# Kernel optimization log

Measured on AMD Instinct MI355X. Metric: run time of the kernel, lower is better.

## Reference

```python
import jax, jax.numpy as jnp
import numpy as np

T, B = 256, 512
IN, NG = 512, 5
H, LAT = 2048, 1024


def gru_cell(x, h, w_ih, w_hh, b_ih, b_hh):
    # torch.nn.GRUCell math
    gi = x @ w_ih.T + b_ih            # [B, 3H]
    gh = h @ w_hh.T + b_hh            # [B, 3H]
    ir, iz, inn = jnp.split(gi, 3, axis=-1)
    hr, hz, hn = jnp.split(gh, 3, axis=-1)
    r = jax.nn.sigmoid(ir + hr)
    z = jax.nn.sigmoid(iz + hz)
    n = jnp.tanh(inn + r * hn)
    return (1.0 - z) * n + z * h


def setup_inputs() -> dict:
    key = jax.random.key(0)
    ks = jax.random.split(key, 20)
    s = 0.02
    d = {
        "x": jax.random.normal(ks[0], (T, B, IN + NG), jnp.float32),
        "latent_genre_vec": jax.random.uniform(ks[1], (B, NG), jnp.float32),
        "eps": jax.random.normal(ks[2], (B, LAT - NG), jnp.float32),
        "enc_w_ih": s * jax.random.normal(ks[3], (3 * H, IN + NG), jnp.float32),
        "enc_w_hh": s * jax.random.normal(ks[4], (3 * H, H), jnp.float32),
        "enc_b_ih": jnp.zeros((3 * H,), jnp.float32),
        "enc_b_hh": jnp.zeros((3 * H,), jnp.float32),
        "dec_w_ih": s * jax.random.normal(ks[5], (3 * H, IN), jnp.float32),
        "dec_w_hh": s * jax.random.normal(ks[6], (3 * H, H), jnp.float32),
        "dec_b_ih": jnp.zeros((3 * H,), jnp.float32),
        "dec_b_hh": jnp.zeros((3 * H,), jnp.float32),
        "fc_mu_w": s * jax.random.normal(ks[7], (LAT - NG, H), jnp.float32),
        "fc_mu_b": jnp.zeros((LAT - NG,), jnp.float32),
        "fc_logvar_w": s * jax.random.normal(ks[8], (LAT - NG, H), jnp.float32),
        "fc_logvar_b": jnp.zeros((LAT - NG,), jnp.float32),
        "fc_output_w": s * jax.random.normal(ks[9], (H, LAT), jnp.float32),
        "fc_output_b": jnp.zeros((H,), jnp.float32),
        "fc_decoder_w": s * jax.random.normal(ks[10], (IN, H), jnp.float32),
        "fc_decoder_b": jnp.zeros((IN,), jnp.float32),
    }
    return d


def reference(x, latent_genre_vec, eps,
              enc_w_ih, enc_w_hh, enc_b_ih, enc_b_hh,
              dec_w_ih, dec_w_hh, dec_b_ih, dec_b_hh,
              fc_mu_w, fc_mu_b, fc_logvar_w, fc_logvar_b,
              fc_output_w, fc_output_b, fc_decoder_w, fc_decoder_b):
    Bsz = x.shape[1]
    h0 = jnp.zeros((Bsz, enc_w_hh.shape[1]), x.dtype)

    # encoder: sequential GRU over time
    def enc_step(h, xt):
        return gru_cell(xt, h, enc_w_ih, enc_w_hh, enc_b_ih, enc_b_hh), None
    h_enc, _ = jax.lax.scan(enc_step, h0, x)

    mu = h_enc @ fc_mu_w.T + fc_mu_b
    logvar = h_enc @ fc_logvar_w.T + fc_logvar_b
    z = mu + jnp.exp(0.5 * logvar) * eps
    z = jnp.concatenate((z, latent_genre_vec), axis=1)
    h_dec0 = z @ fc_output_w.T + fc_output_b

    note0 = jnp.zeros((Bsz, fc_decoder_w.shape[0]), x.dtype)

    def dec_step(carry, _):
        h, note = carry
        h = gru_cell(note, h, dec_w_ih, dec_w_hh, dec_b_ih, dec_b_hh)
        note = h @ fc_decoder_w.T + fc_decoder_b
        return (h, note), note

    _, output = jax.lax.scan(dec_step, (h_dec0, note0), None, length=x.shape[0])
    return output, mu, logvar
```

## Files before the change

kernel.cpp:

```cpp
#include <hip/hip_runtime.h>
#include <hip/hip_bf16.h>

typedef __bf16 bf16_t;
typedef bf16_t bfx8 __attribute__((ext_vector_type(8)));
typedef float  fx4  __attribute__((ext_vector_type(4)));

#define TT     256
#define BB     512
#define INDIM  512
#define NGENRE 5
#define HD     2048
#define LATD   1024
#define LATM   1019
#define XK     517
#define XKP    576
#define CHUNK  64

__device__ __forceinline__ bf16_t f2b(float f) {
  unsigned u = __builtin_bit_cast(unsigned, f);
  u += 0x7fffu + ((u >> 16) & 1u);
  unsigned short s = (unsigned short)(u >> 16);
  return __builtin_bit_cast(bf16_t, s);
}
__device__ __forceinline__ float sigmoidf_(float x) { return 1.0f / (1.0f + __expf(-x)); }

__device__ __forceinline__ void gload16(const bf16_t* g, bf16_t* l) {
  __builtin_amdgcn_global_load_lds((const __attribute__((address_space(1))) void*)g,
                                   (__attribute__((address_space(3))) void*)l,
                                   16, 0, 0);
}
__device__ __forceinline__ void wait_vm0()  { asm volatile("s_waitcnt vmcnt(0)" ::: "memory"); }
__device__ __forceinline__ void wait_vm4()  { asm volatile("s_waitcnt vmcnt(4)" ::: "memory"); }
__device__ __forceinline__ void wait_vm5()  { asm volatile("s_waitcnt vmcnt(5)" ::: "memory"); }
__device__ __forceinline__ void wait_vm6()  { asm volatile("s_waitcnt vmcnt(6)" ::: "memory"); }
__device__ __forceinline__ void wait_vm10() { asm volatile("s_waitcnt vmcnt(10)" ::: "memory"); }
__device__ __forceinline__ void wait_vm12() { asm volatile("s_waitcnt vmcnt(12)" ::: "memory"); }
__device__ __forceinline__ void wait_lgkm0() { asm volatile("s_waitcnt lgkmcnt(0)" ::: "memory"); }

__global__ void wcast_pad(const float* __restrict__ src, bf16_t* __restrict__ dst,
                          int rows_src, int rows_pad, int K, int ldp) {
  for (int r = blockIdx.x; r < rows_pad; r += gridDim.x)
    for (int c = threadIdx.x; c < ldp; c += 256)
      dst[(size_t)r * ldp + c] = (r < rows_src && c < K) ? f2b(src[(size_t)r * K + c]) : f2b(0.0f);
}

__global__ void wtransp(const float* __restrict__ src, bf16_t* __restrict__ dst) {
  int i = blockIdx.x * 256 + threadIdx.x;
  int r = i >> 9, c = i & 511;
  dst[i] = f2b(src[(size_t)c * 2048 + r]);
}
__global__ void bcomp(const float* __restrict__ wih, const float* __restrict__ bdec,
                      float* __restrict__ bc) {
  int r = blockIdx.x * 256 + threadIdx.x;
  if (r >= 3 * HD) return;
  float s = 0.f;
  for (int k = 0; k < 512; ++k) s += wih[(size_t)r * 512 + k] * bdec[k];
  bc[r] = s;
}
__global__ void biasbuild(const float* __restrict__ bc, const float* __restrict__ bih,
                          const float* __restrict__ bhh,
                          float4* __restrict__ bD, float4* __restrict__ bD0) {
  int c = blockIdx.x * 256 + threadIdx.x;
  if (c >= HD) return;
  float r0 = bih[c] + bhh[c];
  float z0 = bih[HD + c] + bhh[HD + c];
  float i0 = bih[2 * HD + c];
  float h0 = bhh[2 * HD + c];
  bD0[c] = float4{r0, z0, i0, h0};
  bD[c]  = float4{r0 + bc[c], z0 + bc[HD + c], i0 + bc[2 * HD + c], h0};
}
__global__ void wprime(const bf16_t* __restrict__ wc, const bf16_t* __restrict__ whh,
                       bf16_t* __restrict__ wp, bf16_t* __restrict__ wp0) {
  const size_t total = (size_t)4 * HD * HD;
  for (size_t i = (size_t)blockIdx.x * 256 + threadIdx.x; i < total; i += (size_t)gridDim.x * 256) {
    int row = (int)(i >> 11), k = (int)(i & 2047);
    int g = row >> 11, j = row & 2047;
    bf16_t v, v0;
    if (g == 0) {
      float a = (float)wc[(size_t)j * HD + k], b = (float)whh[(size_t)j * HD + k];
      v = f2b(a + b); v0 = whh[(size_t)j * HD + k];
    } else if (g == 1) {
      size_t o = (size_t)(HD + j) * HD + k;
      v = f2b((float)wc[o] + (float)whh[o]); v0 = whh[o];
    } else if (g == 2) {
      v = wc[(size_t)(2 * HD + j) * HD + k]; v0 = f2b(0.0f);
    } else {
      v = whh[(size_t)(2 * HD + j) * HD + k]; v0 = v;
    }
    wp[i] = v; wp0[i] = v0;
  }
}

__global__ __launch_bounds__(256, 2)
void gruC(const bf16_t* __restrict__ Hb,
          const bf16_t* __restrict__ Wp,
          const float4* __restrict__ bias4,
          const float* __restrict__ Hin,
          float* __restrict__ Hout, bf16_t* __restrict__ HoutB)
{
  __shared__ bf16_t aT[3][64 * 64];
  __shared__ bf16_t bT[3][128 * 64];
  const int tid = threadIdx.x, wv = tid >> 6, lane = tid & 63;
  const int bid = blockIdx.x;
  const int j0 = (bid & 63) * 32;
  const int m0 = (bid >> 6) * 64;
  const int lr = lane & 15, lk = lane >> 4;
  const int rl = lane >> 3;
  const int cl = (lane & 7) * 8;

  fx4 acc[2][4];
#pragma unroll
  for (int fj = 0; fj < 2; ++fj)
#pragma unroll
    for (int g = 0; g < 4; ++g) acc[fj][g] = fx4{0.f, 0.f, 0.f, 0.f};

  int aOff[2], aSlot[2];
#pragma unroll
  for (int i = 0; i < 2; ++i) {
    const int t = wv * 2 + i;
    const int r = t * 8 + rl;
    const int c = cl ^ ((r & 7) * 8);
    aOff[i] = (m0 + r) * HD + c;
    aSlot[i] = t * 512;
  }
  int bOff[4], bSlot[4];
#pragma unroll
  for (int i = 0; i < 4; ++i) {
    const int t = wv * 4 + i;
    const int r = t * 8 + rl;
    const int g = r >> 5, jj = r & 31;
    const int c = cl ^ ((r & 7) * 8);
    bOff[i] = (g * HD + j0 + jj) * HD + c;
    bSlot[i] = t * 512;
  }
  int aRow, bRow[4][2], ko[2];
  aRow = (wv * 16 + lr) * 64;
#pragma unroll
  for (int g = 0; g < 4; ++g)
#pragma unroll
    for (int fj = 0; fj < 2; ++fj) bRow[g][fj] = (g * 32 + fj * 16 + lr) * 64;
#pragma unroll
  for (int h = 0; h < 2; ++h) ko[h] = (h * 32 + lk * 8) ^ ((lr & 7) * 8);

  auto stage = [&](int buf, int s) {
    const int kb = s * 64;
#pragma unroll
    for (int i = 0; i < 2; ++i) gload16(Hb + aOff[i] + kb, &aT[buf][aSlot[i]]);
#pragma unroll
    for (int i = 0; i < 4; ++i) gload16(Wp + bOff[i] + kb, &bT[buf][bSlot[i]]);
  };

  const int nk = HD / 64;
  stage(0, 0); stage(1, 1);
  int rb = 0, sb = 2;
  for (int s = 0; s < nk; ++s) {
    if (s == nk - 1) wait_vm0(); else wait_vm6();
    __builtin_amdgcn_s_barrier();
    if (s + 2 < nk) stage(sb, s + 2);
    const bf16_t* aB = &aT[rb][0];
    const bf16_t* bB = &bT[rb][0];
    bfx8 af[2]; bfx8 bfr[4][2][2];
#pragma unroll
    for (int h = 0; h < 2; ++h)
      af[h] = *reinterpret_cast<const bfx8*>(&aB[aRow + ko[h]]);
#pragma unroll
    for (int g = 0; g < 4; ++g)
#pragma unroll
      for (int fj = 0; fj < 2; ++fj)
#pragma unroll
        for (int h = 0; h < 2; ++h)
          bfr[g][fj][h] = *reinterpret_cast<const bfx8*>(&bB[bRow[g][fj] + ko[h]]);
    wait_lgkm0();
    __builtin_amdgcn_sched_barrier(0);
    __builtin_amdgcn_s_setprio(1);
#pragma unroll
    for (int h = 0; h < 2; ++h)
#pragma unroll
      for (int g = 0; g < 4; ++g)
#pragma unroll
        for (int fj = 0; fj < 2; ++fj)
          acc[fj][g] = __builtin_amdgcn_mfma_f32_16x16x32_bf16(af[h], bfr[g][fj][h], acc[fj][g], 0, 0, 0);
    __builtin_amdgcn_s_setprio(0);
    rb = (rb == 2) ? 0 : rb + 1;
    sb = (sb == 2) ? 0 : sb + 1;
  }

#pragma unroll
  for (int fj = 0; fj < 2; ++fj) {
    const int col = j0 + fj * 16 + lr;
    const float4 bb = bias4[col];
    const int rbase = m0 + wv * 16 + lk * 4;
#pragma unroll
    for (int q = 0; q < 4; ++q) {
      const int row = rbase + q;
      const float r = sigmoidf_(acc[fj][0][q] + bb.x);
      const float z = sigmoidf_(acc[fj][1][q] + bb.y);
      const float n = tanhf(acc[fj][2][q] + bb.z + r * (acc[fj][3][q] + bb.w));
      const float hv = (1.0f - z) * n + z * Hin[(size_t)row * HD + col];
      Hout[(size_t)row * HD + col]  = hv;
      HoutB[(size_t)row * HD + col] = f2b(hv);
    }
  }
}

__global__ __launch_bounds__(256, 2)
void gru6(const bf16_t* __restrict__ A1, int lda1, int k1s,
          const bf16_t* __restrict__ Wih, int ldwih,
          const bf16_t* __restrict__ Hb,
          const bf16_t* __restrict__ Whh,
          const float* __restrict__ Hin,
          const float* __restrict__ bih, const float* __restrict__ bhh,
          float* __restrict__ Hout, bf16_t* __restrict__ HoutB)
{
  __shared__ bf16_t aT[3][128 * 64];
  __shared__ bf16_t bT[3][48 * 64];
  const int tid = threadIdx.x, wv = tid >> 6, lane = tid & 63;
  const int bid = blockIdx.x;
  const int xcd = bid & 7, loc = bid >> 3;
  const int j0 = (xcd * 16 + (loc >> 2)) * 16;
  const int m0 = (loc & 3) * 128;
  const int lr = lane & 15, lk = lane >> 4;
  const int rl = lane >> 3;
  const int cl = (lane & 7) * 8;

  fx4 acc[2][4];
#pragma unroll
  for (int m = 0; m < 2; ++m)
#pragma unroll
    for (int g = 0; g < 4; ++g) acc[m][g] = fx4{0.f, 0.f, 0.f, 0.f};

  const bf16_t* A1b = A1 ? A1 : Hb;

  int aOff0[4], aOff1[4], aSlot[4];
#pragma unroll
  for (int i = 0; i < 4; ++i) {
    const int t = wv * 4 + i;
    const int r = t * 8 + rl;
    const int c = cl ^ ((r & 7) * 8);
    aOff0[i] = (m0 + r) * lda1 + c;
    aOff1[i] = (m0 + r) * HD + c;
    aSlot[i] = t * 512;
  }
  const int nB  = (wv < 2) ? 2 : 1;
  const int bt0 = (wv < 2) ? wv * 2 : (2 + wv);
  int bOff0[2], bOff1[2], bSlot[2];
#pragma unroll
  for (int i = 0; i < 2; ++i) {
    const int t = bt0 + (i < nB ? i : 0);
    const int r = t * 8 + rl;
    const int g = r >> 4, jj = r & 15;
    const int c = cl ^ ((r & 7) * 8);
    bOff0[i] = (g * HD + j0 + jj) * ldwih + c;
    bOff1[i] = (g * HD + j0 + jj) * HD + c;
    bSlot[i] = t * 512;
  }
  int aRow[2], bRow[3], ko[2];
#pragma unroll
  for (int m = 0; m < 2; ++m) aRow[m] = (wv * 32 + m * 16 + lr) * 64;
#pragma unroll
  for (int g = 0; g < 3; ++g) bRow[g] = (g * 16 + lr) * 64;
#pragma unroll
  for (int h = 0; h < 2; ++h) ko[h] = (h * 32 + lk * 8) ^ ((lr & 7) * 8);

  auto stage = [&](int buf, int s) {
    const bool p = (s >= k1s);
    const int kb = (p ? (s - k1s) : s) * 64;
    bf16_t* aD = &aT[buf][0];
    bf16_t* bD = &bT[buf][0];
    if (p) {
#pragma unroll
      for (int i = 0; i < 4; ++i) gload16(Hb + aOff1[i] + kb, aD + aSlot[i]);
      gload16(Whh + bOff1[0] + kb, bD + bSlot[0]);
      if (wv < 2) gload16(Whh + bOff1[1] + kb, bD + bSlot[1]);
    } else {
#pragma unroll
      for (int i = 0; i < 4; ++i) gload16(A1b + aOff0[i] + kb, aD + aSlot[i]);
      gload16(Wih + bOff0[0] + kb, bD + bSlot[0]);
      if (wv < 2) gload16(Wih + bOff0[1] + kb, bD + bSlot[1]);
    }
  };

  const int nk = k1s + HD / 64;
  stage(0, 0); stage(1, 1); stage(2, 2);
  int buf = 0;
  for (int s = 0; s < nk; ++s) {
    const int rem = nk - 1 - s;
    if (rem >= 2)      { if (wv < 2) wait_vm12(); else wait_vm10(); }
    else if (rem == 1) { if (wv < 2) wait_vm6();  else wait_vm5();  }
    else               wait_vm0();
    __builtin_amdgcn_s_barrier();
    const bf16_t* aB = &aT[buf][0];
    const bf16_t* bB = &bT[buf][0];
    bfx8 af[2][2], bfr[3][2];
#pragma unroll
    for (int m = 0; m < 2; ++m)
#pragma unroll
      for (int h = 0; h < 2; ++h)
        af[m][h] = *reinterpret_cast<const bfx8*>(&aB[aRow[m] + ko[h]]);
#pragma unroll
    for (int g = 0; g < 3; ++g)
#pragma unroll
      for (int h = 0; h < 2; ++h)
        bfr[g][h] = *reinterpret_cast<const bfx8*>(&bB[bRow[g] + ko[h]]);
    wait_lgkm0();
    __builtin_amdgcn_sched_barrier(0);
    __builtin_amdgcn_s_barrier();
    if (s + 3 < nk) stage(buf, s + 3);
    const bool p = (s >= k1s);
    __builtin_amdgcn_s_setprio(1);
#pragma unroll
    for (int h = 0; h < 2; ++h)
#pragma unroll
      for (int g = 0; g < 3; ++g) {
        const int slot = (g == 2) ? (p ? 3 : 2) : g;
#pragma unroll
        for (int m = 0; m < 2; ++m)
          acc[m][slot] = __builtin_amdgcn_mfma_f32_16x16x32_bf16(af[m][h], bfr[g][h], acc[m][slot], 0, 0, 0);
      }
    __builtin_amdgcn_s_setprio(0);
    buf = (buf == 2) ? 0 : buf + 1;
  }

  const int col = j0 + lr;
  const float br  = bih[col] + bhh[col];
  const float bz  = bih[HD + col] + bhh[HD + col];
  const float bin = bih[2 * HD + col];
  const float bhn = bhh[2 * HD + col];
#pragma unroll
  for (int m = 0; m < 2; ++m) {
    const int rbase = m0 + wv * 32 + m * 16 + lk * 4;
#pragma unroll
    for (int q = 0; q < 4; ++q) {
      const int row = rbase + q;
      const float r = sigmoidf_(acc[m][0][q] + br);
      const float z = sigmoidf_(acc[m][1][q] + bz);
      const float n = tanhf(acc[m][2][q] + bin + r * (acc[m][3][q] + bhn));
      const float hv = (1.0f - z) * n + z * Hin[(size_t)row * HD + col];
      Hout[(size_t)row * HD + col]  = hv;
      HoutB[(size_t)row * HD + col] = f2b(hv);
    }
  }
}

__global__ __launch_bounds__(256, 2)
void gemm_nt3(const bf16_t* __restrict__ A, int lda, int K,
              const bf16_t* __restrict__ W, int ldw,
              const float* __restrict__ bias,
              float* __restrict__ O, int ldo, int N,
              bf16_t* __restrict__ OB, int ldob)
{
  __shared__ bf16_t aT[2][64 * 64];
  __shared__ bf16_t bT[2][64 * 64];
  const int tid = threadIdx.x, wave = tid >> 6, lane = tid & 63;
  const int m0 = blockIdx.y * 64, n0 = blockIdx.x * 64;
  const int wm = wave & 1, wn = wave >> 1;
  const int lr = lane & 15, lk = lane >> 4;
  const int rl = lane >> 3, cl = (lane & 7) * 8;

  fx4 acc[2][2];
#pragma unroll
  for (int a = 0; a < 2; ++a)
#pragma unroll
    for (int b = 0; b < 2; ++b) acc[a][b] = fx4{0.f, 0.f, 0.f, 0.f};

  const bf16_t* pA[2]; const bf16_t* pB[2]; int slot[2];
#pragma unroll
  for (int i = 0; i < 2; ++i) {
    const int t = wave * 2 + i;
    const int r = t * 8 + rl;
    const int c = cl ^ ((r & 7) * 8);
    pA[i] = A + (size_t)(m0 + r) * lda + c;
    pB[i] = W + (size_t)(n0 + r) * ldw + c;
    slot[i] = t * 512;
  }
  int aRow[2], bRow[2], ko[2];
#pragma unroll
  for (int f = 0; f < 2; ++f) {
    aRow[f] = (wm * 32 + f * 16 + lr) * 64;
    bRow[f] = (wn * 32 + f * 16 + lr) * 64;
  }
#pragma unroll
  for (int h = 0; h < 2; ++h) ko[h] = (h * 32 + lk * 8) ^ ((lr & 7) * 8);

  auto stage = [&](int buf, int kb) {
#pragma unroll
    for (int i = 0; i < 2; ++i) {
      gload16(pA[i] + kb, &aT[buf][slot[i]]);
      gload16(pB[i] + kb, &bT[buf][slot[i]]);
    }
  };

  const int nk = K >> 6;
  stage(0, 0);
  stage(1, 64);
  for (int s = 0; s < nk; ++s) {
    if (s == nk - 1) wait_vm0(); else wait_vm4();
    __builtin_amdgcn_s_barrier();
    const bf16_t* aB = &aT[s & 1][0];
    const bf16_t* bB = &bT[s & 1][0];
    bfx8 af[2][2], bfr[2][2];
#pragma unroll
    for (int f = 0; f < 2; ++f)
#pragma unroll
      for (int h = 0; h < 2; ++h) {
        af[f][h]  = *reinterpret_cast<const bfx8*>(&aB[aRow[f] + ko[h]]);
        bfr[f][h] = *reinterpret_cast<const bfx8*>(&bB[bRow[f] + ko[h]]);
      }
    wait_lgkm0();
    __builtin_amdgcn_sched_barrier(0);
    __builtin_amdgcn_s_barrier();
    if (s + 2 < nk) stage(s & 1, (s + 2) << 6);
    __builtin_amdgcn_s_setprio(1);
#pragma unroll
    for (int h = 0; h < 2; ++h)
#pragma unroll
      for (int fm = 0; fm < 2; ++fm)
#pragma unroll
        for (int fj = 0; fj < 2; ++fj)
          acc[fm][fj] = __builtin_amdgcn_mfma_f32_16x16x32_bf16(af[fm][h], bfr[fj][h], acc[fm][fj], 0, 0, 0);
    __builtin_amdgcn_s_setprio(0);
  }

#pragma unroll
  for (int fm = 0; fm < 2; ++fm)
#pragma unroll
    for (int fj = 0; fj < 2; ++fj) {
      const int col = n0 + wn * 32 + fj * 16 + lr;
      if (col < N) {
        const float bb = bias[col];
#pragma unroll
        for (int q = 0; q < 4; ++q) {
          const int row = m0 + wm * 32 + fm * 16 + lk * 4 + q;
          const float v = acc[fm][fj][q] + bb;
          O[(size_t)row * ldo + col] = v;
          if (OB) OB[(size_t)row * ldob + col] = f2b(v);
        }
      }
    }
}

__global__ void build_zb(const float* __restrict__ mu, const float* __restrict__ lv,
                         const float* __restrict__ eps, const float* __restrict__ genre,
                         bf16_t* __restrict__ zb) {
  int i = blockIdx.x * 256 + threadIdx.x;
  int b = i >> 10, c = i & 1023;
  float v;
  if (c < LATM) {
    size_t k = (size_t)b * LATM + c;
    v = mu[k] + expf(0.5f * lv[k]) * eps[k];
  } else {
    v = genre[b * NGENRE + (c - LATM)];
  }
  zb[i] = f2b(v);
}

__global__ __launch_bounds__(256, 1)
void gru_stepF(const float* __restrict__ A1, int lda1, int K1,
               const float* __restrict__ Wih,
               const float* __restrict__ Hin,
               const float* __restrict__ Whh,
               const float* __restrict__ bih, const float* __restrict__ bhh,
               float* __restrict__ Hout)
{
  __shared__ bf16_t a_lds[128][32];
  __shared__ bf16_t b_lds[96][32];
  const int tid = threadIdx.x, wave = tid >> 6, lane = tid & 63;
  const int m0 = (blockIdx.x >> 6) * 128, j0 = (blockIdx.x & 63) * 32;
  const int lr = lane & 15, lk = lane >> 4;
  fx4 acc[2][2][4];
#pragma unroll
  for (int a = 0; a < 2; ++a)
#pragma unroll
    for (int b = 0; b < 2; ++b)
#pragma unroll
      for (int g = 0; g < 4; ++g) acc[a][b][g] = fx4{0.f, 0.f, 0.f, 0.f};

  for (int ph = 0; ph < 2; ++ph) {
    const float* Ag = ph ? Hin : A1;
    const int lda = ph ? HD : lda1, kLen = ph ? HD : K1;
    const float* W = ph ? Whh : Wih;
    const int nslot = ph ? 3 : 2;
    const int nkk = (kLen + 31) >> 5;
    for (int s = 0; s < nkk; ++s) {
      const int kb = s << 5;
#pragma unroll
      for (int it = 0; it < 16; ++it) {
        int i = tid + it * 256;
        int r = i >> 5, kk = i & 31, gk = kb + kk;
        float v = 0.0f;
        if (Ag && gk < kLen) v = Ag[(size_t)(m0 + r) * lda + gk];
        a_lds[r][kk] = f2b(v);
      }
#pragma unroll
      for (int it = 0; it < 12; ++it) {
        int i = tid + it * 256;
        int r = i >> 5, kk = i & 31, g = r >> 5, jj = r & 31, gk = kb + kk;
        b_lds[r][kk] = (gk < kLen) ? f2b(W[(size_t)(g * HD + j0 + jj) * kLen + gk]) : f2b(0.0f);
      }
      __syncthreads();
      bfx8 af[2];
#pragma unroll
      for (int fm = 0; fm < 2; ++fm)
        af[fm] = *reinterpret_cast<const bfx8*>(&a_lds[wave * 32 + fm * 16 + lr][lk * 8]);
#pragma unroll
      for (int g = 0; g < 3; ++g) {
        const int slot = (g == 2) ? nslot : g;
#pragma unroll
        for (int fj = 0; fj < 2; ++fj) {
          bfx8 bfr = *reinterpret_cast<const bfx8*>(&b_lds[g * 32 + fj * 16 + lr][lk * 8]);
#pragma unroll
          for (int fm = 0; fm < 2; ++fm)
            acc[fm][fj][slot] = __builtin_amdgcn_mfma_f32_16x16x32_bf16(af[fm], bfr, acc[fm][fj][slot], 0, 0, 0);
        }
      }
      __syncthreads();
    }
  }
#pragma unroll
  for (int fj = 0; fj < 2; ++fj) {
    const int col = j0 + fj * 16 + lr;
    const float br = bih[col] + bhh[col];
    const float bz = bih[HD + col] + bhh[HD + col];
    const float bin = bih[2 * HD + col];
    const float bhn = bhh[2 * HD + col];
#pragma unroll
    for (int fm = 0; fm < 2; ++fm) {
      const int rbase = m0 + wave * 32 + fm * 16 + lk * 4;
#pragma unroll
      for (int q = 0; q < 4; ++q) {
        const int row = rbase + q;
        const float r = sigmoidf_(acc[fm][fj][0][q] + br);
        const float z = sigmoidf_(acc[fm][fj][1][q] + bz);
        const float n = tanhf(acc[fm][fj][2][q] + bin + r * (acc[fm][fj][3][q] + bhn));
        Hout[(size_t)row * HD + col] = (1.0f - z) * n + z * Hin[(size_t)row * HD + col];
      }
    }
  }
}

__global__ __launch_bounds__(256, 1)
void gemm_ntF(const float* __restrict__ A, int lda, int K,
              const float* __restrict__ W,
              const float* __restrict__ bias,
              float* __restrict__ O, int ldo, int N)
{
  __shared__ bf16_t a_lds[64][32];
  __shared__ bf16_t b_lds[64][32];
  const int tid = threadIdx.x, wave = tid >> 6, lane = tid & 63;
  const int m0 = blockIdx.y * 64, n0 = blockIdx.x * 64;
  const int wm = (wave & 1) * 32, wn = (wave >> 1) * 32;
  const int lr = lane & 15, lk = lane >> 4;
  fx4 acc[2][2];
#pragma unroll
  for (int a = 0; a < 2; ++a)
#pragma unroll
    for (int b = 0; b < 2; ++b) acc[a][b] = fx4{0.f, 0.f, 0.f, 0.f};
  for (int kb = 0; kb < K; kb += 32) {
#pragma unroll
    for (int it = 0; it < 8; ++it) {
      int i = tid + it * 256;
      int r = i >> 5, kk = i & 31;
      a_lds[r][kk] = f2b(A[(size_t)(m0 + r) * lda + kb + kk]);
    }
#pragma unroll
    for (int it = 0; it < 8; ++it) {
      int i = tid + it * 256;
      int r = i >> 5, kk = i & 31;
      int n = n0 + r;
      b_lds[r][kk] = (n < N) ? f2b(W[(size_t)n * K + kb + kk]) : f2b(0.0f);
    }
    __syncthreads();
    bfx8 af[2], bfr[2];
#pragma unroll
    for (int f = 0; f < 2; ++f) {
      af[f] = *reinterpret_cast<const bfx8*>(&a_lds[wm + f * 16 + lr][lk * 8]);
      bfr[f] = *reinterpret_cast<const bfx8*>(&b_lds[wn + f * 16 + lr][lk * 8]);
    }
#pragma unroll
    for (int fm = 0; fm < 2; ++fm)
#pragma unroll
      for (int fj = 0; fj < 2; ++fj)
        acc[fm][fj] = __builtin_amdgcn_mfma_f32_16x16x32_bf16(af[fm], bfr[fj], acc[fm][fj], 0, 0, 0);
    __syncthreads();
  }
#pragma unroll
  for (int fm = 0; fm < 2; ++fm)
#pragma unroll
    for (int fj = 0; fj < 2; ++fj) {
      const int col = n0 + wn + fj * 16 + lr;
      if (col < N) {
        const float bb = bias[col];
#pragma unroll
        for (int q = 0; q < 4; ++q) {
          const int row = m0 + wm + fm * 16 + lk * 4 + q;
          O[(size_t)row * ldo + col] = acc[fm][fj][q] + bb;
        }
      }
    }
}

__global__ void build_zf(const float* __restrict__ mu, const float* __restrict__ lv,
                         const float* __restrict__ eps, const float* __restrict__ genre,
                         float* __restrict__ z) {
  int i = blockIdx.x * 256 + threadIdx.x;
  int b = i >> 10, c = i & 1023;
  z[i] = (c < LATM) ? mu[(size_t)b * LATM + c] + expf(0.5f * lv[(size_t)b * LATM + c]) * eps[(size_t)b * LATM + c]
                    : genre[b * NGENRE + (c - LATM)];
}

extern "C" void kernel_launch(void* const* d_in, const int* in_sizes, int n_in,
                              void* d_out, int out_size, void* d_ws, size_t ws_size,
                              hipStream_t stream) {
  const float* x      = (const float*)d_in[0];
  const float* genre  = (const float*)d_in[1];
  const float* eps    = (const float*)d_in[2];
  const float* eWih   = (const float*)d_in[3];
  const float* eWhh   = (const float*)d_in[4];
  const float* eBih   = (const float*)d_in[5];
  const float* eBhh   = (const float*)d_in[6];
  const float* dWih   = (const float*)d_in[7];
  const float* dWhh   = (const float*)d_in[8];
  const float* dBih   = (const float*)d_in[9];
  const float* dBhh   = (const float*)d_in[10];
  const float* fcMuW  = (const float*)d_in[11];
  const float* fcMuB  = (const float*)d_in[12];
  const float* fcLvW  = (const float*)d_in[13];
  const float* fcLvB  = (const float*)d_in[14];
  const float* fcOutW = (const float*)d_in[15];
  const float* fcOutB = (const float*)d_in[16];
  const float* fcDecW = (const float*)d_in[17];
  const float* fcDecB = (const float*)d_in[18];

  float* out = (float*)d_out;
  float* muO = out + (size_t)TT * BB * INDIM;
  float* lvO = muO + (size_t)BB * LATM;

  const size_t nEih = (size_t)3 * HD * XKP;
  const size_t nEhh = (size_t)3 * HD * HD;
  const size_t nDih = (size_t)3 * HD * INDIM;
  const size_t nDhh = (size_t)3 * HD * HD;
  const size_t nMu  = (size_t)1024 * HD;
  const size_t nOut = (size_t)HD * LATD;
  const size_t nDec = (size_t)INDIM * HD;
  const size_t oEih = 0;
  const size_t oEhh = oEih + nEih;
  const size_t oDih = oEhh + nEhh;
  const size_t oDhh = oDih + nDih;
  const size_t oMu  = oDhh + nDhh;
  const size_t oLv  = oMu + nMu;
  const size_t oOut = oLv + nMu;
  const size_t oDec = oOut + nOut;
  const size_t wTot = oDec + nDec;

  const size_t bytesW  = wTot * 2;
  const size_t bytesHF = (size_t)BB * HD * 4;
  const size_t bytesHB = (size_t)BB * HD * 2;
  const size_t bytesZB = (size_t)BB * LATD * 2;
  const size_t bytesNB = (size_t)BB * INDIM * 2;
  const size_t bytesX1 = (size_t)BB * XKP * 2;
  const size_t bytesXB = (size_t)TT * BB * XKP * 2;
  const size_t needB = bytesW + 2 * bytesHF + 2 * bytesHB + bytesZB + bytesNB + bytesX1 + 1024;
  const size_t needA = needB + bytesXB;
  const size_t bytesWdT  = (size_t)HD * 512 * 2;
  const size_t bytesWcB  = (size_t)3 * HD * HD * 2;
  const size_t bytesWcF  = (size_t)3 * HD * HD * 4;
  const size_t bytesWp   = (size_t)4 * HD * HD * 2;
  const size_t bytesBc   = (size_t)3 * HD * 4;
  const size_t bytesB4   = (size_t)HD * 16;
  const size_t bytesZero = (size_t)HD * 4;
  const size_t bytesHist = (size_t)CHUNK * BB * HD * 2;
  const size_t needC = needA + bytesWdT + bytesWcB + bytesWcF + 2 * bytesWp +
                       bytesBc + 2 * bytesB4 + bytesZero + bytesHist + 1024;

  if (ws_size >= needB) {
    const bool haveXB = (ws_size >= needA);
    const bool haveCP = (ws_size >= needC);
    char* p = (char*)d_ws;
    bf16_t* wb = (bf16_t*)p;            p += bytesW;
    float* h0  = (float*)p;             p += bytesHF;
    float* h1  = (float*)p;             p += bytesHF;
    bf16_t* hb0 = (bf16_t*)p;           p += bytesHB;
    bf16_t* hb1 = (bf16_t*)p;           p += bytesHB;
    bf16_t* zb  = (bf16_t*)p;           p += bytesZB;
    bf16_t* nb  = (bf16_t*)p;           p += bytesNB;
    bf16_t* x1  = (bf16_t*)p;           p += bytesX1;
    bf16_t* xb  = haveXB ? (bf16_t*)p : nullptr;
    if (haveXB) p += bytesXB;
    bf16_t *wdT = nullptr, *wcB = nullptr, *wP = nullptr, *wP0 = nullptr, *hist = nullptr;
    float *wcF = nullptr, *bc = nullptr, *zerosb = nullptr;
    float4 *b4D = nullptr, *b4D0 = nullptr;
    if (haveCP) {
      wdT = (bf16_t*)p;  p += bytesWdT;
      wcB = (bf16_t*)p;  p += bytesWcB;
      wP  = (bf16_t*)p;  p += bytesWp;
      wP0 = (bf16_t*)p;  p += bytesWp;
      wcF = (float*)p;   p += bytesWcF;
      bc  = (float*)p;   p += bytesBc;
      b4D = (float4*)p;  p += bytesB4;
      b4D0 = (float4*)p; p += bytesB4;
      zerosb = (float*)p; p += bytesZero;
      hist = (bf16_t*)p; p += bytesHist;
    }

    auto cast = [&](const float* s, bf16_t* d, int rs, int rp, int K, int ldp) {
      int g = rp > 8192 ? 8192 : rp;
      wcast_pad<<<g, 256, 0, stream>>>(s, d, rs, rp, K, ldp);
    };
    cast(eWih,   wb + oEih, 3 * HD, 3 * HD, XK,    XKP);
    cast(eWhh,   wb + oEhh, 3 * HD, 3 * HD, HD,    HD);
    cast(dWih,   wb + oDih, 3 * HD, 3 * HD, INDIM, INDIM);
    cast(dWhh,   wb + oDhh, 3 * HD, 3 * HD, HD,    HD);
    cast(fcMuW,  wb + oMu,  LATM,   1024,   HD,    HD);
    cast(fcLvW,  wb + oLv,  LATM,   1024,   HD,    HD);
    cast(fcOutW, wb + oOut, HD,     HD,     LATD,  LATD);
    cast(fcDecW, wb + oDec, INDIM,  INDIM,  HD,    HD);
    if (haveXB) cast(x, xb, TT * BB, TT * BB, XK, XKP);

    if (haveCP) {
      hipMemsetAsync(zerosb, 0, bytesZero, stream);
      wtransp<<<(HD * 512) / 256, 256, 0, stream>>>(fcDecW, wdT);
      gemm_nt3<<<dim3(HD / 64, (3 * HD) / 64), 256, 0, stream>>>(
          wb + oDih, INDIM, INDIM, wdT, INDIM, zerosb, wcF, HD, HD, wcB, HD);
      bcomp<<<(3 * HD) / 256, 256, 0, stream>>>(dWih, fcDecB, bc);
      biasbuild<<<HD / 256, 256, 0, stream>>>(bc, dBih, dBhh, b4D, b4D0);
      wprime<<<4096, 256, 0, stream>>>(wcB, wb + oDhh, wP, wP0);
    }

    hipMemsetAsync(h0, 0, bytesHF, stream);
    hipMemsetAsync(hb0, 0, bytesHB, stream);

    float*  hF[2] = {h0, h1};
    bf16_t* hB[2] = {hb0, hb1};

    for (int t = 0; t < TT; ++t) {
      const int ci = t & 1, co = ci ^ 1;
      const bf16_t* xt;
      if (haveXB) {
        xt = xb + (size_t)t * BB * XKP;
      } else {
        wcast_pad<<<512, 256, 0, stream>>>(x + (size_t)t * BB * XK, x1, BB, BB, XK, XKP);
        xt = x1;
      }
      gru6<<<512, 256, 0, stream>>>(xt, XKP, XKP / 64,
                                    wb + oEih, XKP, hB[ci], wb + oEhh,
                                    hF[ci], eBih, eBhh, hF[co], hB[co]);
    }
    gemm_nt3<<<dim3(16, 8), 256, 0, stream>>>(hB[0], HD, HD, wb + oMu, HD, fcMuB,
                                              muO, LATM, LATM, nullptr, 0);
    gemm_nt3<<<dim3(16, 8), 256, 0, stream>>>(hB[0], HD, HD, wb + oLv, HD, fcLvB,
                                              lvO, LATM, LATM, nullptr, 0);
    build_zb<<<(BB * LATD) / 256, 256, 0, stream>>>(muO, lvO, eps, genre, zb);
    gemm_nt3<<<dim3(32, 8), 256, 0, stream>>>(zb, LATD, LATD, wb + oOut, LATD, fcOutB,
                                              hF[0], HD, HD, hB[0], HD);
    if (haveCP) {
      for (int t = 0; t < TT; ++t) {
        const bf16_t* hprev = (t == 0) ? hB[0] : hist + (size_t)((t - 1) & (CHUNK - 1)) * BB * HD;
        gruC<<<512, 256, 0, stream>>>(hprev, t ? wP : wP0, t ? b4D : b4D0,
                                      hF[t & 1], hF[(t & 1) ^ 1],
                                      hist + (size_t)(t & (CHUNK - 1)) * BB * HD);
        if ((t & (CHUNK - 1)) == CHUNK - 1) {
          gemm_nt3<<<dim3(INDIM / 64, (CHUNK * BB) / 64), 256, 0, stream>>>(
              hist, HD, HD, wb + oDec, HD, fcDecB,
              out + (size_t)(t - (CHUNK - 1)) * BB * INDIM, INDIM, INDIM, nullptr, 0);
        }
      }
    } else {
      for (int t = 0; t < TT; ++t) {
        const int ci = t & 1, co = ci ^ 1;
        gru6<<<512, 256, 0, stream>>>(t ? nb : (const bf16_t*)nullptr, INDIM,
                                      t ? INDIM / 64 : 0,
                                      wb + oDih, INDIM, hB[ci], wb + oDhh,
                                      hF[ci], dBih, dBhh, hF[co], hB[co]);
        gemm_nt3<<<dim3(8, 8), 256, 0, stream>>>(hB[co], HD, HD, wb + oDec, HD, fcDecB,
                                                 out + (size_t)t * BB * INDIM, INDIM, INDIM,
                                                 nb, INDIM);
      }
    }
  } else {
    float* h0 = (float*)d_ws;
    float* h1 = h0 + (size_t)BB * HD;
    float* zb = h1 + (size_t)BB * HD;
    hipMemsetAsync(h0, 0, (size_t)BB * HD * sizeof(float), stream);
    float* hF[2] = {h0, h1};
    for (int t = 0; t < TT; ++t) {
      const int ci = t & 1, co = ci ^ 1;
      gru_stepF<<<256, 256, 0, stream>>>(x + (size_t)t * BB * XK, XK, XK, eWih,
                                         hF[ci], eWhh, eBih, eBhh, hF[co]);
    }
    gemm_ntF<<<dim3(16, 8), 256, 0, stream>>>(hF[0], HD, HD, fcMuW, fcMuB, muO, LATM, LATM);
    gemm_ntF<<<dim3(16, 8), 256, 0, stream>>>(hF[0], HD, HD, fcLvW, fcLvB, lvO, LATM, LATM);
    build_zf<<<(BB * LATD) / 256, 256, 0, stream>>>(muO, lvO, eps, genre, zb);
    gemm_ntF<<<dim3(32, 8), 256, 0, stream>>>(zb, LATD, LATD, fcOutW, fcOutB, hF[0], HD, HD);
    for (int t = 0; t < TT; ++t) {
      const int ci = t & 1, co = ci ^ 1;
      gru_stepF<<<256, 256, 0, stream>>>(t ? out + (size_t)(t - 1) * BB * INDIM : nullptr,
                                         INDIM, INDIM, dWih, hF[ci], dWhh, dBih, dBhh, hF[co]);
      gemm_ntF<<<dim3(8, 8), 256, 0, stream>>>(hF[co], HD, HD, fcDecW, fcDecB,
                                               out + (size_t)t * BB * INDIM, INDIM, INDIM);
    }
  }
  (void)in_sizes; (void)n_in; (void)out_size;
}
```

Before: 17.12 ms.

## Precompute encoder input projections in one GEMM and retile decoder GRU kernel

Hoists the encoder's x@W_ih projection out of the time loop into a single large batched GEMM whose bf16 results are stored in the workspace. A new per-step kernel then only multiplies by W_hh and adds the precomputed gates. The decoder recurrent kernel is also retiled so each wave owns output columns rather than rows, with the gate epilogue staged through LDS. The encoder path needs a large extra workspace and stores the input gates in bf16.

New measurement: 17.04 ms. No clear change (-0.4%).

```diff
diff --git a/kernel.cpp b/kernel.cpp
--- a/kernel.cpp
+++ b/kernel.cpp
@@ -15,6 +15,7 @@
 #define XK     517
 #define XKP    576
 #define CHUNK  64
+#define GIW    6144
 
 __device__ __forceinline__ bf16_t f2b(float f) {
   unsigned u = __builtin_bit_cast(unsigned, f);
@@ -92,11 +93,11 @@
 }
 
 __global__ __launch_bounds__(256, 2)
-void gruC(const bf16_t* __restrict__ Hb,
-          const bf16_t* __restrict__ Wp,
-          const float4* __restrict__ bias4,
-          const float* __restrict__ Hin,
-          float* __restrict__ Hout, bf16_t* __restrict__ HoutB)
+void gruC2(const bf16_t* __restrict__ Hb,
+           const bf16_t* __restrict__ Wp,
+           const float4* __restrict__ bias4,
+           const float* __restrict__ Hin,
+           float* __restrict__ Hout, bf16_t* __restrict__ HoutB)
 {
   __shared__ bf16_t aT[3][64 * 64];
   __shared__ bf16_t bT[3][128 * 64];
@@ -108,11 +109,11 @@
   const int rl = lane >> 3;
   const int cl = (lane & 7) * 8;
 
-  fx4 acc[2][4];
-#pragma unroll
-  for (int fj = 0; fj < 2; ++fj)
-#pragma unroll
-    for (int g = 0; g < 4; ++g) acc[fj][g] = fx4{0.f, 0.f, 0.f, 0.f};
+  fx4 acc[4][2];
+#pragma unroll
+  for (int m = 0; m < 4; ++m)
+#pragma unroll
+    for (int fj = 0; fj < 2; ++fj) acc[m][fj] = fx4{0.f, 0.f, 0.f, 0.f};
 
   int aOff[2], aSlot[2];
 #pragma unroll
@@ -133,12 +134,11 @@
     bOff[i] = (g * HD + j0 + jj) * HD + c;
     bSlot[i] = t * 512;
   }
-  int aRow, bRow[4][2], ko[2];
-  aRow = (wv * 16 + lr) * 64;
-#pragma unroll
-  for (int g = 0; g < 4; ++g)
-#pragma unroll
-    for (int fj = 0; fj < 2; ++fj) bRow[g][fj] = (g * 32 + fj * 16 + lr) * 64;
+  int aRow[4], bRow[2], ko[2];
+#pragma unroll
+  for (int m = 0; m < 4; ++m) aRow[m] = (m * 16 + lr) * 64;
+#pragma unroll
+  for (int fj = 0; fj < 2; ++fj) bRow[fj] = (wv * 32 + fj * 16 + lr) * 64;
 #pragma unroll
   for (int h = 0; h < 2; ++h) ko[h] = (h * 32 + lk * 8) ^ ((lr & 7) * 8);
 
@@ -159,46 +159,181 @@
     if (s + 2 < nk) stage(sb, s + 2);
     const bf16_t* aB = &aT[rb][0];
     const bf16_t* bB = &bT[rb][0];
-    bfx8 af[2]; bfx8 bfr[4][2][2];
-#pragma unroll
-    for (int h = 0; h < 2; ++h)
-      af[h] = *reinterpret_cast<const bfx8*>(&aB[aRow + ko[h]]);
-#pragma unroll
-    for (int g = 0; g < 4; ++g)
-#pragma unroll
-      for (int fj = 0; fj < 2; ++fj)
-#pragma unroll
-        for (int h = 0; h < 2; ++h)
-          bfr[g][fj][h] = *reinterpret_cast<const bfx8*>(&bB[bRow[g][fj] + ko[h]]);
+    bfx8 af[4][2], bfr[2][2];
+#pragma unroll
+    for (int m = 0; m < 4; ++m)
+#pragma unroll
+      for (int h = 0; h < 2; ++h)
+        af[m][h] = *reinterpret_cast<const bfx8*>(&aB[aRow[m] + ko[h]]);
+#pragma unroll
+    for (int fj = 0; fj < 2; ++fj)
+#pragma unroll
+      for (int h = 0; h < 2; ++h)
+        bfr[fj][h] = *reinterpret_cast<const bfx8*>(&bB[bRow[fj] + ko[h]]);
     wait_lgkm0();
     __builtin_amdgcn_sched_barrier(0);
     __builtin_amdgcn_s_setprio(1);
 #pragma unroll
     for (int h = 0; h < 2; ++h)
 #pragma unroll
-      for (int g = 0; g < 4; ++g)
+      for (int m = 0; m < 4; ++m)
 #pragma unroll
         for (int fj = 0; fj < 2; ++fj)
-          acc[fj][g] = __builtin_amdgcn_mfma_f32_16x16x32_bf16(af[h], bfr[g][fj][h], acc[fj][g], 0, 0, 0);
+          acc[m][fj] = __builtin_amdgcn_mfma_f32_16x16x32_bf16(af[m][h], bfr[fj][h], acc[m][fj], 0, 0, 0);
     __builtin_amdgcn_s_setprio(0);
     rb = (rb == 2) ? 0 : rb + 1;
     sb = (sb == 2) ? 0 : sb + 1;
   }
 
-#pragma unroll
-  for (int fj = 0; fj < 2; ++fj) {
-    const int col = j0 + fj * 16 + lr;
-    const float4 bb = bias4[col];
-    const int rbase = m0 + wv * 16 + lk * 4;
+  __syncthreads();
+  float* eL = (float*)&bT[0][0];
+#pragma unroll
+  for (int m = 0; m < 4; ++m)
+#pragma unroll
+    for (int fj = 0; fj < 2; ++fj)
+#pragma unroll
+      for (int q = 0; q < 4; ++q)
+        eL[((wv * 64 + m * 16 + lk * 4 + q) * 33 + fj * 16 + lr)] = acc[m][fj][q];
+  __syncthreads();
+  const int col = lane & 31;
+  const int rh  = lane >> 5;
+  const float4 bb = bias4[j0 + col];
+#pragma unroll
+  for (int i = 0; i < 8; ++i) {
+    const int rowL = wv * 16 + rh * 8 + i;
+    const float e0 = eL[((0 * 64 + rowL) * 33 + col)];
+    const float e1 = eL[((1 * 64 + rowL) * 33 + col)];
+    const float e2 = eL[((2 * 64 + rowL) * 33 + col)];
+    const float e3 = eL[((3 * 64 + rowL) * 33 + col)];
+    const float r = sigmoidf_(e0 + bb.x);
+    const float z = sigmoidf_(e1 + bb.y);
+    const float n = tanhf(e2 + bb.z + r * (e3 + bb.w));
+    const size_t o = (size_t)(m0 + rowL) * HD + j0 + col;
+    const float hv = (1.0f - z) * n + z * Hin[o];
+    Hout[o]  = hv;
+    HoutB[o] = f2b(hv);
+  }
+}
+
+__global__ __launch_bounds__(256, 2)
+void gruE(const bf16_t* __restrict__ gi,
+          const bf16_t* __restrict__ Hb,
+          const bf16_t* __restrict__ Whh,
+          const float* __restrict__ Hin,
+          const float* __restrict__ bih, const float* __restrict__ bhh,
+          float* __restrict__ Hout, bf16_t* __restrict__ HoutB)
+{
+  __shared__ bf16_t aT[3][64 * 64];
+  __shared__ bf16_t bT[3][96 * 64];
+  const int tid = threadIdx.x, wv = tid >> 6, lane = tid & 63;
+  const int mh = wv >> 1, ch = wv & 1;
+  const int bid = blockIdx.x;
+  const int j0 = (bid & 63) * 32;
+  const int m0 = (bid >> 6) * 64;
+  const int lr = lane & 15, lk = lane >> 4;
+  const int rl = lane >> 3;
+  const int cl = (lane & 7) * 8;
+  const int colG = j0 + ch * 16 + lr;
+
+  fx4 acc[2][3];
+#pragma unroll
+  for (int m = 0; m < 2; ++m) {
 #pragma unroll
     for (int q = 0; q < 4; ++q) {
-      const int row = rbase + q;
-      const float r = sigmoidf_(acc[fj][0][q] + bb.x);
-      const float z = sigmoidf_(acc[fj][1][q] + bb.y);
-      const float n = tanhf(acc[fj][2][q] + bb.z + r * (acc[fj][3][q] + bb.w));
-      const float hv = (1.0f - z) * n + z * Hin[(size_t)row * HD + col];
-      Hout[(size_t)row * HD + col]  = hv;
-      HoutB[(size_t)row * HD + col] = f2b(hv);
+      const int row = m0 + mh * 32 + m * 16 + lk * 4 + q;
+      acc[m][0][q] = (float)gi[(size_t)row * GIW + colG];
+      acc[m][1][q] = (float)gi[(size_t)row * GIW + 2048 + colG];
+      acc[m][2][q] = 0.0f;
+    }
+  }
+
+  int aOff[2], aSlot[2];
+#pragma unroll
+  for (int i = 0; i < 2; ++i) {
+    const int t = wv * 2 + i;
+    const int r = t * 8 + rl;
+    const int c = cl ^ ((r & 7) * 8);
+    aOff[i] = (m0 + r) * HD + c;
+    aSlot[i] = t * 512;
+  }
+  int bOff[3], bSlot[3];
+#pragma unroll
+  for (int i = 0; i < 3; ++i) {
+    const int t = wv * 3 + i;
+    const int r = t * 8 + rl;
+    const int g = r >> 5, jj = r & 31;
+    const int c = cl ^ ((r & 7) * 8);
+    bOff[i] = (g * HD + j0 + jj) * HD + c;
+    bSlot[i] = t * 512;
+  }
+  int aRow[2], bRow[3], ko[2];
+#pragma unroll
+  for (int m = 0; m < 2; ++m) aRow[m] = (mh * 32 + m * 16 + lr) * 64;
+#pragma unroll
+  for (int g = 0; g < 3; ++g) bRow[g] = (g * 32 + ch * 16 + lr) * 64;
+#pragma unroll
+  for (int h = 0; h < 2; ++h) ko[h] = (h * 32 + lk * 8) ^ ((lr & 7) * 8);
+
+  auto stage = [&](int buf, int s) {
+    const int kb = s * 64;
+#pragma unroll
+    for (int i = 0; i < 2; ++i) gload16(Hb + aOff[i] + kb, &aT[buf][aSlot[i]]);
+#pragma unroll
+    for (int i = 0; i < 3; ++i) gload16(Whh + bOff[i] + kb, &bT[buf][bSlot[i]]);
+  };
+
+  const int nk = HD / 64;
+  stage(0, 0); stage(1, 1);
+  int rb = 0, sb = 2;
+  for (int s = 0; s < nk; ++s) {
+    if (s == nk - 1) wait_vm0(); else wait_vm5();
+    __builtin_amdgcn_s_barrier();
+    if (s + 2 < nk) stage(sb, s + 2);
+    const bf16_t* aB = &aT[rb][0];
+    const bf16_t* bB = &bT[rb][0];
+    bfx8 af[2][2], bfr[3][2];
+#pragma unroll
+    for (int m = 0; m < 2; ++m)
+#pragma unroll
+      for (int h = 0; h < 2; ++h)
+        af[m][h] = *reinterpret_cast<const bfx8*>(&aB[aRow[m] + ko[h]]);
+#pragma unroll
+    for (int g = 0; g < 3; ++g)
+#pragma unroll
+      for (int h = 0; h < 2; ++h)
+        bfr[g][h] = *reinterpret_cast<const bfx8*>(&bB[bRow[g] + ko[h]]);
+    wait_lgkm0();
+    __builtin_amdgcn_sched_barrier(0);
+    __builtin_amdgcn_s_setprio(1);
+#pragma unroll
+    for (int h = 0; h < 2; ++h)
+#pragma unroll
+      for (int g = 0; g < 3; ++g)
+#pragma unroll
+        for (int m = 0; m < 2; ++m)
+          acc[m][g] = __builtin_amdgcn_mfma_f32_16x16x32_bf16(af[m][h], bfr[g][h], acc[m][g], 0, 0, 0);
+    __builtin_amdgcn_s_setprio(0);
+    rb = (rb == 2) ? 0 : rb + 1;
+    sb = (sb == 2) ? 0 : sb + 1;
+  }
+
+  const float br  = bih[colG] + bhh[colG];
+  const float bz  = bih[HD + colG] + bhh[HD + colG];
+  const float bin = bih[2 * HD + colG];
+  const float bhn = bhh[2 * HD + colG];
+#pragma unroll
+  for (int m = 0; m < 2; ++m) {
+#pragma unroll
+    for (int q = 0; q < 4; ++q) {
+      const int row = m0 + mh * 32 + m * 16 + lk * 4 + q;
+      const float gin = (float)gi[(size_t)row * GIW + 4096 + colG];
+      const float r = sigmoidf_(acc[m][0][q] + br);
+      const float z = sigmoidf_(acc[m][1][q] + bz);
+      const float n = tanhf(gin + bin + r * (acc[m][2][q] + bhn));
+      const size_t o = (size_t)row * HD + colG;
+      const float hv = (1.0f - z) * n + z * Hin[o];
+      Hout[o]  = hv;
+      HoutB[o] = f2b(hv);
     }
   }
 }
@@ -432,7 +567,7 @@
         for (int q = 0; q < 4; ++q) {
           const int row = m0 + wm * 32 + fm * 16 + lk * 4 + q;
           const float v = acc[fm][fj][q] + bb;
-          O[(size_t)row * ldo + col] = v;
+          if (O)  O[(size_t)row * ldo + col] = v;
           if (OB) OB[(size_t)row * ldob + col] = f2b(v);
         }
       }
@@ -667,14 +802,17 @@
   const size_t bytesWp   = (size_t)4 * HD * HD * 2;
   const size_t bytesBc   = (size_t)3 * HD * 4;
   const size_t bytesB4   = (size_t)HD * 16;
-  const size_t bytesZero = (size_t)HD * 4;
+  const size_t bytesZero = (size_t)GIW * 4;
   const size_t bytesHist = (size_t)CHUNK * BB * HD * 2;
   const size_t needC = needA + bytesWdT + bytesWcB + bytesWcF + 2 * bytesWp +
                        bytesBc + 2 * bytesB4 + bytesZero + bytesHist + 1024;
+  const size_t bytesGi = (size_t)TT * BB * GIW * 2;
+  const size_t needD = needC + bytesGi;
 
   if (ws_size >= needB) {
     const bool haveXB = (ws_size >= needA);
     const bool haveCP = (ws_size >= needC);
+    const bool haveGI = (ws_size >= needD);
     char* p = (char*)d_ws;
     bf16_t* wb = (bf16_t*)p;            p += bytesW;
     float* h0  = (float*)p;             p += bytesHF;
@@ -689,6 +827,7 @@
     bf16_t *wdT = nullptr, *wcB = nullptr, *wP = nullptr, *wP0 = nullptr, *hist = nullptr;
     float *wcF = nullptr, *bc = nullptr, *zerosb = nullptr;
     float4 *b4D = nullptr, *b4D0 = nullptr;
+    bf16_t *gix = nullptr;
     if (haveCP) {
       wdT = (bf16_t*)p;  p += bytesWdT;
       wcB = (bf16_t*)p;  p += bytesWcB;
@@ -701,6 +840,7 @@
       zerosb = (float*)p; p += bytesZero;
       hist = (bf16_t*)p; p += bytesHist;
     }
+    if (haveGI) { gix = (bf16_t*)p; p += bytesGi; }
 
     auto cast = [&](const float* s, bf16_t* d, int rs, int rp, int K, int ldp) {
       int g = rp > 8192 ? 8192 : rp;
@@ -725,6 +865,10 @@
       biasbuild<<<HD / 256, 256, 0, stream>>>(bc, dBih, dBhh, b4D, b4D0);
       wprime<<<4096, 256, 0, stream>>>(wcB, wb + oDhh, wP, wP0);
     }
+    if (haveGI) {
+      gemm_nt3<<<dim3(GIW / 64, (TT * BB) / 64), 256, 0, stream>>>(
+          xb, XKP, XKP, wb + oEih, XKP, zerosb, nullptr, 0, GIW, gix, GIW);
+    }
 
     hipMemsetAsync(h0, 0, bytesHF, stream);
     hipMemsetAsync(hb0, 0, bytesHB, stream);
@@ -732,18 +876,26 @@
     float*  hF[2] = {h0, h1};
     bf16_t* hB[2] = {hb0, hb1};
 
-    for (int t = 0; t < TT; ++t) {
-      const int ci = t & 1, co = ci ^ 1;
-      const bf16_t* xt;
-      if (haveXB) {
-        xt = xb + (size_t)t * BB * XKP;
-      } else {
-        wcast_pad<<<512, 256, 0, stream>>>(x + (size_t)t * BB * XK, x1, BB, BB, XK, XKP);
-        xt = x1;
-      }
-      gru6<<<512, 256, 0, stream>>>(xt, XKP, XKP / 64,
-                                    wb + oEih, XKP, hB[ci], wb + oEhh,
-                                    hF[ci], eBih, eBhh, hF[co], hB[co]);
+    if (haveGI) {
+      for (int t = 0; t < TT; ++t) {
+        const int ci = t & 1, co = ci ^ 1;
+        gruE<<<512, 256, 0, stream>>>(gix + (size_t)t * BB * GIW, hB[ci], wb + oEhh,
+                                      hF[ci], eBih, eBhh, hF[co], hB[co]);
+      }
+    } else {
+      for (int t = 0; t < TT; ++t) {
+        const int ci = t & 1, co = ci ^ 1;
+        const bf16_t* xt;
+        if (haveXB) {
+          xt = xb + (size_t)t * BB * XKP;
+        } else {
+          wcast_pad<<<512, 256, 0, stream>>>(x + (size_t)t * BB * XK, x1, BB, BB, XK, XKP);
+          xt = x1;
+        }
+        gru6<<<512, 256, 0, stream>>>(xt, XKP, XKP / 64,
+                                      wb + oEih, XKP, hB[ci], wb + oEhh,
+                                      hF[ci], eBih, eBhh, hF[co], hB[co]);
+      }
     }
     gemm_nt3<<<dim3(16, 8), 256, 0, stream>>>(hB[0], HD, HD, wb + oMu, HD, fcMuB,
                                               muO, LATM, LATM, nullptr, 0);
@@ -755,9 +907,9 @@
     if (haveCP) {
       for (int t = 0; t < TT; ++t) {
         const bf16_t* hprev = (t == 0) ? hB[0] : hist + (size_t)((t - 1) & (CHUNK - 1)) * BB * HD;
-        gruC<<<512, 256, 0, stream>>>(hprev, t ? wP : wP0, t ? b4D : b4D0,
-                                      hF[t & 1], hF[(t & 1) ^ 1],
-                                      hist + (size_t)(t & (CHUNK - 1)) * BB * HD);
+        gruC2<<<512, 256, 0, stream>>>(hprev, t ? wP : wP0, t ? b4D : b4D0,
+                                       hF[t & 1], hF[(t & 1) ^ 1],
+                                       hist + (size_t)(t & (CHUNK - 1)) * BB * HD);
         if ((t & (CHUNK - 1)) == CHUNK - 1) {
           gemm_nt3<<<dim3(INDIM / 64, (CHUNK * BB) / 64), 256, 0, stream>>>(
               hist, HD, HD, wb + oDec, HD, fcDecB,
```
